# Optimization experiments

Hardware: AMD Instinct MI355X
Metric: run time of the kernel (lower is better)

The kernel has to match this reference:

```python
import jax, jax.numpy as jnp
import numpy as np

B, T, D_IN = 32, 1024, 80
SHAPES = (512, 512, 256)
WIN = 2          # delta window
H = 256          # LSTM hidden units (per direction)
LSTM_IN = SHAPES[-1] * 3


def setup_inputs() -> dict:
    key = jax.random.key(0)
    ks = jax.random.split(key, 20)
    inp = {}
    inp["x"] = jax.random.normal(ks[0], (B, T, D_IN), dtype=jnp.float32)
    lens = jax.random.randint(ks[1], (B,), T // 2, T + 1)
    inp["x_lengths"] = lens.at[0].set(T)  # ensure max length == T (static output shape)
    dims = (D_IN,) + SHAPES
    for i in range(len(SHAPES)):
        s = 1.0 / np.sqrt(dims[i])
        inp[f"enc_W{i}"] = jax.random.uniform(ks[2 + i], (dims[i + 1], dims[i]), minval=-s, maxval=s, dtype=jnp.float32)
        inp[f"enc_b{i}"] = jax.random.uniform(ks[5 + i], (dims[i + 1],), minval=-s, maxval=s, dtype=jnp.float32)
    s = 1.0 / np.sqrt(H)
    for d, name in enumerate(("f", "b")):
        inp[f"W_ih_{name}"] = jax.random.uniform(ks[8 + 4 * d], (4 * H, LSTM_IN), minval=-s, maxval=s, dtype=jnp.float32)
        inp[f"W_hh_{name}"] = jax.random.uniform(ks[9 + 4 * d], (4 * H, H), minval=-s, maxval=s, dtype=jnp.float32)
        inp[f"b_ih_{name}"] = jax.random.uniform(ks[10 + 4 * d], (4 * H,), minval=-s, maxval=s, dtype=jnp.float32)
        inp[f"b_hh_{name}"] = jax.random.uniform(ks[11 + 4 * d], (4 * H,), minval=-s, maxval=s, dtype=jnp.float32)
    # init_hidden() in torch uses randn; fix it here as deterministic inputs. [2 dirs, B, H]
    inp["h0"] = jax.random.normal(ks[16], (2, B, H), dtype=jnp.float32)
    inp["c0"] = jax.random.normal(ks[17], (2, B, H), dtype=jnp.float32)
    return inp


def _deltas(x, w):
    # edge-replicated window, z[:,t] = sum_j (y[t+w+j]-y[t+w-j])/(2j)
    Tt = x.shape[1]
    y = jnp.concatenate([jnp.repeat(x[:, :1], w, axis=1), x, jnp.repeat(x[:, -1:], w, axis=1)], axis=1)
    z = jnp.zeros_like(x)
    for j in range(1, w + 1):
        z = z + (y[:, w + j:w + j + Tt] - y[:, w - j:w - j + Tt]) / (2.0 * j)
    return z


def _lstm(xs, h0, c0, Wih, Whh, b):
    # xs: [T, B, F] -> hs: [T, B, H]; torch gate order i,f,g,o
    def step(carry, xt):
        h, c = carry
        g = xt @ Wih.T + h @ Whh.T + b
        i, f, gg, o = jnp.split(g, 4, axis=-1)
        c = jax.nn.sigmoid(f) * c + jax.nn.sigmoid(i) * jnp.tanh(gg)
        h = jax.nn.sigmoid(o) * jnp.tanh(c)
        return (h, c), h
    _, hs = jax.lax.scan(step, (h0, c0), xs)
    return hs


def _forward(x, x_lengths, enc_W0, enc_b0, enc_W1, enc_b1, enc_W2, enc_b2,
             W_ih_f, W_hh_f, b_ih_f, b_hh_f, W_ih_b, W_hh_b, b_ih_b, b_hh_b, h0, c0):
    # MLP encoder with ReLU after every layer
    h = x
    for Wm, bm in ((enc_W0, enc_b0), (enc_W1, enc_b1), (enc_W2, enc_b2)):
        h = jax.nn.relu(h @ Wm.T + bm)
    d1 = _deltas(h, WIN)
    d2 = _deltas(d1, WIN)
    feat = jnp.concatenate([h, d1, d2], axis=2)  # [B, T, 3*shapes[-1]]
    # sort by length descending (pack_padded_sequence)
    order = jnp.argsort(-x_lengths)
    lens = x_lengths[order]
    feat = feat[order]
    t_idx = jnp.arange(T)
    # forward direction
    hf = _lstm(jnp.swapaxes(feat, 0, 1), h0[0], c0[0], W_ih_f, W_hh_f, b_ih_f + b_hh_f)
    hf = jnp.swapaxes(hf, 0, 1)  # [B, T, H]
    # backward direction: reverse valid part of each sequence (packed semantics)
    rev = jnp.clip(lens[:, None] - 1 - t_idx[None, :], 0, T - 1)  # [B, T]
    x_rev = jnp.take_along_axis(feat, rev[:, :, None], axis=1)
    hb = _lstm(jnp.swapaxes(x_rev, 0, 1), h0[1], c0[1], W_ih_b, W_hh_b, b_ih_b + b_hh_b)
    hb = jnp.take_along_axis(jnp.swapaxes(hb, 0, 1), rev[:, :, None], axis=1)
    # pad_packed_sequence zeros out padded steps
    mask = (t_idx[None, :] < lens[:, None])[:, :, None]
    out = jnp.where(mask, jnp.concatenate([hf, hb], axis=2), 0.0)
    return out, order


def reference(x, x_lengths, enc_W0, enc_b0, enc_W1, enc_b1, enc_W2, enc_b2,
              W_ih_f, W_hh_f, b_ih_f, b_hh_f, W_ih_b, W_hh_b, b_ih_b, b_hh_b, h0, c0):
    return _forward(x, x_lengths, enc_W0, enc_b0, enc_W1, enc_b1, enc_W2, enc_b2,
                    W_ih_f, W_hh_f, b_ih_f, b_hh_f, W_ih_b, W_hh_b, b_ih_b, b_hh_b, h0, c0)
```

## Files before the change

### kernel.cpp

```cpp
#include <hip/hip_runtime.h>
#include <cstdint>
#include <cstddef>

#define B_SZ 32
#define T_SZ 1024
#define DIN  80
#define H3   256
#define FEAT 768
#define G4   1024
#define HH   256

typedef __attribute__((ext_vector_type(8))) short short8;
typedef __attribute__((ext_vector_type(4))) float f32x4;
typedef __attribute__((ext_vector_type(8))) int v8i;

__device__ inline float bf2f(unsigned short u) {
    return __uint_as_float(((unsigned int)u) << 16);
}
__device__ inline unsigned short f2bf(float f) {
    unsigned int u = __float_as_uint(f);
    u += 0x7fffu + ((u >> 16) & 1u);
    return (unsigned short)(u >> 16);
}
#define LOG2E 1.4426950408889634f
__device__ inline float sigm(float x) {
    return __builtin_amdgcn_rcpf(1.f + __builtin_amdgcn_exp2f(x * -LOG2E));
}
__device__ inline float tanh_f(float x) {
    return fmaf(2.f, __builtin_amdgcn_rcpf(1.f + __builtin_amdgcn_exp2f(x * (-2.f * LOG2E))), -1.f);
}

__device__ inline void gld16(const void* g, void* l) {
    __builtin_amdgcn_global_load_lds(
        (const __attribute__((address_space(1))) unsigned int*)g,
        (__attribute__((address_space(3))) unsigned int*)l, 16, 0, 0);
}

__device__ inline void cvt_seg(const float* __restrict__ s, unsigned short* __restrict__ d,
                               int n4, int i, int stride) {
    for (int k = i; k < n4; k += stride) {
        float4 f = ((const float4*)(const void*)s)[k];
        ushort4 u;
        u.x = f2bf(f.x); u.y = f2bf(f.y); u.z = f2bf(f.z); u.w = f2bf(f.w);
        ((ushort4*)(void*)d)[k] = u;
    }
}

__global__ void k_cvt4(const float* __restrict__ src, unsigned short* __restrict__ dst, int n4) {
    int i = blockIdx.x * 256 + threadIdx.x;
    cvt_seg(src, dst, n4, i, gridDim.x * 256);
}

__global__ void k_cvtw(const float* __restrict__ s0, unsigned short* __restrict__ d0,
                       const float* __restrict__ s1, unsigned short* __restrict__ d1,
                       const float* __restrict__ s2, unsigned short* __restrict__ d2,
                       const float* __restrict__ s3, unsigned short* __restrict__ d3,
                       const float* __restrict__ s4, unsigned short* __restrict__ d4) {
    int i = blockIdx.x * 256 + threadIdx.x;
    int stride = gridDim.x * 256;
    cvt_seg(s0, d0, 10240,  i, stride);
    cvt_seg(s1, d1, 65536,  i, stride);
    cvt_seg(s2, d2, 32768,  i, stride);
    cvt_seg(s3, d3, 196608, i, stride);
    cvt_seg(s4, d4, 196608, i, stride);
}

__global__ void k_order(const int* __restrict__ lens, int* __restrict__ order,
                        int* __restrict__ lens_sorted, float* __restrict__ out_order) {
    int b = threadIdx.x;
    if (b < B_SZ) {
        int lb = lens[b];
        int r = 0;
        for (int j = 0; j < B_SZ; ++j) {
            int lj = lens[j];
            if (lj > lb || (lj == lb && j < b)) ++r;
        }
        order[r] = b;
        lens_sorted[r] = lb;
        out_order[r] = (float)b;
    }
}

__global__ void k_ztail(const int* __restrict__ lens_sorted, float* __restrict__ out) {
    int t = blockIdx.x, bs = blockIdx.y;
    if (t < lens_sorted[bs]) return;
    float4* p = (float4*)(out + ((size_t)bs * T_SZ + t) * 512);
    p[threadIdx.x] = make_float4(0.f, 0.f, 0.f, 0.f);
}

__global__ void k_wfrag8(const float* __restrict__ Whhf, const float* __restrict__ Whhb,
                         unsigned char* __restrict__ dst) {
    int t = blockIdx.x * 256 + threadIdx.x;
    int dir = t >> 14;
    t &= 16383;
    const float* Whh = dir ? Whhb : Whhf;
    unsigned char* d = dst + (size_t)dir * 262144;
    int lane = t & 63, hf = (t >> 6) & 1, kc = (t >> 7) & 1, nt = t >> 8;
    int l16 = lane & 15;
    int gb = nt >> 4, m = nt & 15, wv = m >> 1, pp = m & 1;
    int n = gb * 256 + wv * 32 + l16 * 2 + pp;
    int k0 = kc * 128 + (lane >> 4) * 32 + hf * 16;
    const float* p = Whh + (size_t)n * 256 + k0;
    unsigned int o[4];
    #pragma unroll
    for (int q = 0; q < 4; ++q) {
        float4 f = *(const float4*)(const void*)(p + 4 * q);
        o[q] = (__builtin_amdgcn_cvt_pk_fp8_f32(f.x, f.y, 0, false) & 0xffff)
             | (__builtin_amdgcn_cvt_pk_fp8_f32(f.z, f.w, 0, false) << 16);
    }
    int slot = (nt * 2 + kc) * 64 + lane;
    *(uint4*)(void*)(d + (size_t)slot * 32 + hf * 16) = make_uint4(o[0], o[1], o[2], o[3]);
}

__global__ __launch_bounds__(256) void k_gemm(
    const unsigned short* __restrict__ A, const unsigned short* __restrict__ Bw,
    const float* __restrict__ bias1, const float* __restrict__ bias2,
    unsigned short* __restrict__ C, int M, int N, int K, int relu)
{
    int tid  = threadIdx.x;
    int lane = tid & 63;
    int wave = tid >> 6;
    int waveM = wave >> 1, waveN = wave & 1;
    int l16  = lane & 15;
    int quad = lane >> 4;
    int mBase = blockIdx.x * 32 + waveM * 16;
    int nBase = blockIdx.y * 128 + waveN * 64;

    const unsigned short* pA  = A  + (size_t)(mBase + l16) * K + quad * 8;
    const unsigned short* pB0 = Bw + (size_t)(nBase +  0 + l16) * K + quad * 8;
    const unsigned short* pB1 = Bw + (size_t)(nBase + 16 + l16) * K + quad * 8;
    const unsigned short* pB2 = Bw + (size_t)(nBase + 32 + l16) * K + quad * 8;
    const unsigned short* pB3 = Bw + (size_t)(nBase + 48 + l16) * K + quad * 8;

    const short8 z8 = {0, 0, 0, 0, 0, 0, 0, 0};
    f32x4 acc0 = {0.f, 0.f, 0.f, 0.f};
    f32x4 acc1 = acc0, acc2 = acc0, acc3 = acc0;

    for (int k0 = 0; k0 < K; k0 += 32) {
        bool ok = (k0 + quad * 8) < K;
        short8 av  = ok ? *(const short8*)(const void*)(pA  + k0) : z8;
        short8 bv0 = ok ? *(const short8*)(const void*)(pB0 + k0) : z8;
        short8 bv1 = ok ? *(const short8*)(const void*)(pB1 + k0) : z8;
        short8 bv2 = ok ? *(const short8*)(const void*)(pB2 + k0) : z8;
        short8 bv3 = ok ? *(const short8*)(const void*)(pB3 + k0) : z8;
        acc0 = __builtin_amdgcn_mfma_f32_16x16x32_bf16(av, bv0, acc0, 0, 0, 0);
        acc1 = __builtin_amdgcn_mfma_f32_16x16x32_bf16(av, bv1, acc1, 0, 0, 0);
        acc2 = __builtin_amdgcn_mfma_f32_16x16x32_bf16(av, bv2, acc2, 0, 0, 0);
        acc3 = __builtin_amdgcn_mfma_f32_16x16x32_bf16(av, bv3, acc3, 0, 0, 0);
    }

    int rowD = mBase + quad * 4;
    #pragma unroll
    for (int nt = 0; nt < 4; ++nt) {
        int col = nBase + nt * 16 + l16;
        float bsum = 0.f;
        if (bias1) bsum += bias1[col];
        if (bias2) bsum += bias2[col];
        f32x4 a = (nt == 0) ? acc0 : (nt == 1) ? acc1 : (nt == 2) ? acc2 : acc3;
        #pragma unroll
        for (int r = 0; r < 4; ++r) {
            float v = a[r] + bsum;
            if (relu) v = v > 0.f ? v : 0.f;
            C[(size_t)(rowD + r) * N + col] = f2bf(v);
        }
    }
}

__global__ __launch_bounds__(256) void k_gemm_t(
    const unsigned short* __restrict__ A, const unsigned short* __restrict__ Bw,
    const float* __restrict__ bias1, const float* __restrict__ bias2,
    unsigned short* __restrict__ C, int N, int K, int relu)
{
    __shared__ unsigned short lA[128 * 32];
    __shared__ unsigned short lB[128 * 32];
    int tid  = threadIdx.x;
    int lane = tid & 63;
    int wave = tid >> 6;
    int l16  = lane & 15, quad = lane >> 4;
    int wm = wave >> 1, wn = wave & 1;
    size_t mBase = (size_t)blockIdx.y * 128;
    size_t nBase = (size_t)blockIdx.x * 128;

    int c0 = tid, c1 = tid + 256;
    const unsigned short* sA0 = A  + (mBase + (c0 >> 2)) * K + (c0 & 3) * 8;
    const unsigned short* sA1 = A  + (mBase + (c1 >> 2)) * K + (c1 & 3) * 8;
    const unsigned short* sB0 = Bw + (nBase + (c0 >> 2)) * K + (c0 & 3) * 8;
    const unsigned short* sB1 = Bw + (nBase + (c1 >> 2)) * K + (c1 & 3) * 8;
    unsigned short* dA0 = lA + c0 * 8;
    unsigned short* dA1 = lA + c1 * 8;
    unsigned short* dB0 = lB + c0 * 8;
    unsigned short* dB1 = lB + c1 * 8;

    f32x4 acc[4][4];
    #pragma unroll
    for (int i = 0; i < 4; ++i)
        #pragma unroll
        for (int j = 0; j < 4; ++j) acc[i][j] = (f32x4){0.f, 0.f, 0.f, 0.f};

    const unsigned short* la = lA + (wm * 64 + l16) * 32 + quad * 8;
    const unsigned short* lb = lB + (wn * 64 + l16) * 32 + quad * 8;

    for (int k0 = 0; k0 < K; k0 += 32) {
        gld16(sA0 + k0, dA0);
        gld16(sA1 + k0, dA1);
        gld16(sB0 + k0, dB0);
        gld16(sB1 + k0, dB1);
        __syncthreads();
        short8 af[4], bf[4];
        #pragma unroll
        for (int i = 0; i < 4; ++i) {
            af[i] = *(const short8*)(const void*)(la + i * 16 * 32);
            bf[i] = *(const short8*)(const void*)(lb + i * 16 * 32);
        }
        #pragma unroll
        for (int i = 0; i < 4; ++i)
            #pragma unroll
            for (int j = 0; j < 4; ++j)
                acc[i][j] = __builtin_amdgcn_mfma_f32_16x16x32_bf16(af[i], bf[j], acc[i][j], 0, 0, 0);
        __syncthreads();
    }

    #pragma unroll
    for (int j = 0; j < 4; ++j) {
        int col = (int)nBase + wn * 64 + j * 16 + l16;
        float bsum = 0.f;
        if (bias1) bsum += bias1[col];
        if (bias2) bsum += bias2[col];
        #pragma unroll
        for (int i = 0; i < 4; ++i) {
            int row = (int)mBase + wm * 64 + i * 16 + quad * 4;
            #pragma unroll
            for (int r = 0; r < 4; ++r) {
                float v = acc[i][j][r] + bsum;
                if (relu) v = v > 0.f ? v : 0.f;
                C[(size_t)(row + r) * N + col] = f2bf(v);
            }
        }
    }
}

__global__ void k_deltas(const unsigned short* __restrict__ hbuf, const int* __restrict__ order,
                         unsigned short* __restrict__ feat)
{
    int bt = blockIdx.x;
    int c  = threadIdx.x;
    int bs = bt >> 10, t = bt & 1023;
    int b  = order[bs];
    const unsigned short* hb = hbuf + (size_t)b * T_SZ * H3 + c;

    float hv[9];
    #pragma unroll
    for (int d = -4; d <= 4; ++d) {
        int tt = t + d;
        tt = tt < 0 ? 0 : (tt > T_SZ - 1 ? T_SZ - 1 : tt);
        hv[d + 4] = bf2f(hb[(size_t)tt * H3]);
    }
    float d1v[5];
    #pragma unroll
    for (int s = -2; s <= 2; ++s) {
        d1v[s + 2] = (hv[s + 5] - hv[s + 3]) * 0.5f + (hv[s + 6] - hv[s + 2]) * 0.25f;
    }
    int sp1 = (t + 1 > T_SZ - 1 ? T_SZ - 1 : t + 1) - t;
    int sm1 = (t - 1 < 0 ? 0 : t - 1) - t;
    int sp2 = (t + 2 > T_SZ - 1 ? T_SZ - 1 : t + 2) - t;
    int sm2 = (t - 2 < 0 ? 0 : t - 2) - t;
    float d2 = (d1v[2 + sp1] - d1v[2 + sm1]) * 0.5f + (d1v[2 + sp2] - d1v[2 + sm2]) * 0.25f;

    size_t fb = (size_t)bt * FEAT;
    feat[fb + c]       = hb[(size_t)t * H3];
    feat[fb + 256 + c] = f2bf(d1v[2]);
    feat[fb + 512 + c] = f2bf(d2);
}

__global__ __launch_bounds__(512, 2) void k_lstm_fp8(
    const unsigned short* __restrict__ g3f, const unsigned short* __restrict__ g3b,
    const unsigned char* __restrict__ wfrag8,
    const float* __restrict__ h0, const float* __restrict__ c0,
    const int* __restrict__ lens_sorted, float* __restrict__ out)
{
    int rq = blockIdx.x, dir = blockIdx.y;
    const unsigned short* g3 = (dir ? g3b : g3f) + (size_t)rq * 4194304;
    const unsigned char* wsrc = wfrag8 + (size_t)dir * 262144;

    __shared__ __align__(16) unsigned char hA[2][4096];

    int tid = threadIdx.x;
    int wave = tid >> 6, lane = tid & 63;
    int l16 = lane & 15, quad = lane >> 4;

    v8i regB[4][2][2];
    #pragma unroll
    for (int gb = 0; gb < 4; ++gb)
        #pragma unroll
        for (int p = 0; p < 2; ++p)
            #pragma unroll
            for (int kc = 0; kc < 2; ++kc) {
                int nt = gb * 16 + 2 * wave + p;
                regB[gb][p][kc] = *(const v8i*)(const void*)
                    (wsrc + ((size_t)((nt * 2 + kc) * 64 + lane)) * 32);
            }

    for (int i = tid; i < 2048; i += 512) ((unsigned int*)(void*)hA)[i] = 0;
    __syncthreads();
    for (int i = tid; i < 1024; i += 512) {
        int b = i >> 8, c = i & 255;
        float hv = h0[(size_t)dir * B_SZ * HH + (size_t)(rq * 4 + b) * HH + c];
        hA[0][(c >> 7) * 2048 + (((c >> 5) & 3) * 16 + 4 * b) * 32 + (c & 31)] =
            (unsigned char)(__builtin_amdgcn_cvt_pk_fp8_f32(hv, hv, 0, false) & 0xff);
    }

    int grow = rq * 4 + quad;
    int elen = lens_sorted[grow];
    int maxlen = lens_sorted[rq * 4];
    int col0 = 32 * wave + 2 * l16;
    float2 cini = *(const float2*)(const void*)
        (c0 + (size_t)dir * B_SZ * HH + (size_t)grow * HH + col0);
    float c2[2] = {cini.x, cini.y};
    float* out_r = out + (size_t)grow * T_SZ * 512 + dir * HH + col0;
    const unsigned short* gbase0 = g3 + ((size_t)quad << 20) + col0;
    int woff = (col0 >> 7) * 2048 + (((col0 >> 5) & 3) * 16 + 4 * quad) * 32 + (col0 & 31);

    {
        int tr0 = dir ? (elen - 1) : 0;
        const unsigned short* rp = gbase0 + ((size_t)tr0 << 10);
        unsigned int t0 = *(const unsigned int*)(const void*)(rp);
        unsigned int t1 = *(const unsigned int*)(const void*)(rp + 256);
        unsigned int t2 = *(const unsigned int*)(const void*)(rp + 512);
        unsigned int t3 = *(const unsigned int*)(const void*)(rp + 768);
        __syncthreads();

        unsigned int gI = t0, gF = t1, gG = t2, gO = t3;
        const f32x4 zf = {0.f, 0.f, 0.f, 0.f};

        for (int s = 0; s < maxlen; ++s) {
            const unsigned char* Ab = hA[s & 1];
            v8i a0 = *(const v8i*)(const void*)(Ab + lane * 32);
            v8i a1 = *(const v8i*)(const void*)(Ab + 2048 + lane * 32);

            int trn = dir ? (elen - 2 - s) : (s + 1);
            trn = trn < 0 ? 0 : (trn > T_SZ - 1 ? T_SZ - 1 : trn);
            const unsigned short* rn = gbase0 + ((size_t)trn << 10);
            unsigned int nI = *(const unsigned int*)(const void*)(rn);
            unsigned int nF = *(const unsigned int*)(const void*)(rn + 256);
            unsigned int nG = *(const unsigned int*)(const void*)(rn + 512);
            unsigned int nO = *(const unsigned int*)(const void*)(rn + 768);

            f32x4 acc[4][2];
            #pragma unroll
            for (int gb = 0; gb < 4; ++gb)
                #pragma unroll
                for (int p = 0; p < 2; ++p)
                    acc[gb][p] = __builtin_amdgcn_mfma_scale_f32_16x16x128_f8f6f4(
                        a0, regB[gb][p][0], zf, 0, 0, 0, 0x7F7F7F7F, 0, 0x7F7F7F7F);
            #pragma unroll
            for (int gb = 0; gb < 4; ++gb)
                #pragma unroll
                for (int p = 0; p < 2; ++p)
                    acc[gb][p] = __builtin_amdgcn_mfma_scale_f32_16x16x128_f8f6f4(
                        a1, regB[gb][p][1], acc[gb][p], 0, 0, 0, 0x7F7F7F7F, 0, 0x7F7F7F7F);

            float tc[2];
            #pragma unroll
            for (int p = 0; p < 2; ++p) {
                float iv = acc[0][p][0] + bf2f((unsigned short)(p ? (gI >> 16) : (gI & 0xffffu)));
                float fv = acc[1][p][0] + bf2f((unsigned short)(p ? (gF >> 16) : (gF & 0xffffu)));
                float gv = acc[2][p][0] + bf2f((unsigned short)(p ? (gG >> 16) : (gG & 0xffffu)));
                c2[p] = sigm(fv) * c2[p] + sigm(iv) * tanh_f(gv);
                tc[p] = tanh_f(c2[p]);
            }
            float ov0 = acc[3][0][0] + bf2f((unsigned short)(gO & 0xffffu));
            float ov1 = acc[3][1][0] + bf2f((unsigned short)(gO >> 16));
            float hv0 = sigm(ov0) * tc[0];
            float hv1 = sigm(ov1) * tc[1];

            unsigned short pk = (unsigned short)
                (__builtin_amdgcn_cvt_pk_fp8_f32(hv0, hv1, 0, false) & 0xffffu);
            *(unsigned short*)(void*)(hA[(s + 1) & 1] + woff) = pk;
            if (s < elen) {
                int t_out = dir ? (elen - 1 - s) : s;
                *(float2*)(void*)(out_r + (size_t)t_out * 512) = make_float2(hv0, hv1);
            }
            gI = nI; gF = nF; gG = nG; gO = nO;
            asm volatile("s_waitcnt lgkmcnt(0)" ::: "memory");
            __builtin_amdgcn_s_barrier();
        }
    }
}

#define OFF_XBF    ((size_t)0)
#define OFF_A0     ((size_t)5242880)
#define OFF_A1     ((size_t)38797312)
#define OFF_HBUF   ((size_t)72351744)
#define OFF_FEAT   ((size_t)89128960)
#define OFF_GF     OFF_A0
#define OFF_GB     ((size_t)139460608)
#define OFF_W0     ((size_t)206569472)
#define OFF_W1     ((size_t)206651392)
#define OFF_W2     ((size_t)207175680)
#define OFF_WIHF   ((size_t)207437824)
#define OFF_WIHB   ((size_t)209010688)
#define OFF_WFRAG  ((size_t)210583552)
#define OFF_ORDER  ((size_t)212680704)
#define OFF_LENS   ((size_t)212680832)

extern "C" void kernel_launch(void* const* d_in, const int* in_sizes, int n_in,
                              void* d_out, int out_size, void* d_ws, size_t ws_size,
                              hipStream_t stream)
{
    const float* x    = (const float*)d_in[0];
    const int*   xlen = (const int*)d_in[1];
    const float* eW0  = (const float*)d_in[2];
    const float* eb0  = (const float*)d_in[3];
    const float* eW1  = (const float*)d_in[4];
    const float* eb1  = (const float*)d_in[5];
    const float* eW2  = (const float*)d_in[6];
    const float* eb2  = (const float*)d_in[7];
    const float* Wihf = (const float*)d_in[8];
    const float* Whhf = (const float*)d_in[9];
    const float* bihf = (const float*)d_in[10];
    const float* bhhf = (const float*)d_in[11];
    const float* Wihb = (const float*)d_in[12];
    const float* Whhb = (const float*)d_in[13];
    const float* bihb = (const float*)d_in[14];
    const float* bhhb = (const float*)d_in[15];
    const float* h0   = (const float*)d_in[16];
    const float* c0   = (const float*)d_in[17];
    float* out = (float*)d_out;

    char* ws = (char*)d_ws;
    unsigned short* xbf    = (unsigned short*)(ws + OFF_XBF);
    unsigned short* a0     = (unsigned short*)(ws + OFF_A0);
    unsigned short* a1     = (unsigned short*)(ws + OFF_A1);
    unsigned short* hbuf   = (unsigned short*)(ws + OFF_HBUF);
    unsigned short* feat   = (unsigned short*)(ws + OFF_FEAT);
    unsigned short* gatesF = (unsigned short*)(ws + OFF_GF);
    unsigned short* gatesB = (unsigned short*)(ws + OFF_GB);
    unsigned short* w0     = (unsigned short*)(ws + OFF_W0);
    unsigned short* w1     = (unsigned short*)(ws + OFF_W1);
    unsigned short* w2     = (unsigned short*)(ws + OFF_W2);
    unsigned short* wihf   = (unsigned short*)(ws + OFF_WIHF);
    unsigned short* wihb   = (unsigned short*)(ws + OFF_WIHB);
    unsigned char*  wfrag8 = (unsigned char*)(ws + OFF_WFRAG);
    int* order             = (int*)(ws + OFF_ORDER);
    int* lens_sorted       = (int*)(ws + OFF_LENS);

    k_cvt4<<<1024, 256, 0, stream>>>(x, xbf, B_SZ * T_SZ * DIN / 4);
    k_cvtw<<<512, 256, 0, stream>>>(eW0, w0, eW1, w1, eW2, w2, Wihf, wihf, Wihb, wihb);
    k_wfrag8<<<128, 256, 0, stream>>>(Whhf, Whhb, wfrag8);
    k_order<<<1, 64, 0, stream>>>(xlen, order, lens_sorted, out + (size_t)B_SZ * T_SZ * 512);
    k_ztail<<<dim3(T_SZ, B_SZ), 128, 0, stream>>>(lens_sorted, out);

    k_gemm<<<dim3(1024, 4), 256, 0, stream>>>(xbf, w0, nullptr, eb0, a0, 32768, 512, 80, 1);
    k_gemm_t<<<dim3(4, 256), 256, 0, stream>>>(a0, w1, eb1, nullptr, a1,   512, 512, 1);
    k_gemm_t<<<dim3(2, 256), 256, 0, stream>>>(a1, w2, eb2, nullptr, hbuf, 256, 512, 1);

    k_deltas<<<32768, 256, 0, stream>>>(hbuf, order, feat);

    k_gemm_t<<<dim3(8, 256), 256, 0, stream>>>(feat, wihf, bihf, bhhf, gatesF, 1024, 768, 0);
    k_gemm_t<<<dim3(8, 256), 256, 0, stream>>>(feat, wihb, bihb, bhhb, gatesB, 1024, 768, 0);

    k_lstm_fp8<<<dim3(8, 2), 512, 0, stream>>>(gatesF, gatesB, wfrag8, h0, c0,
                                               lens_sorted, out);
}
```

Baseline: 1.236 ms.

## Widen LSTM recurrence to 1024 threads and merge setup and input-gate GEMMs

The recurrent LSTM kernel now runs 16 waves per block, each owning one 16-column tile per gate instead of two. The precomputed input gates are fed in as the MFMA accumulator initialiser rather than added afterwards. The Whh fragment layout is simplified to match the new per-wave ownership. The x conversion, bias summation and length sorting are folded into one setup kernel, and the forward and backward input-projection GEMMs run as a single launch over N=2048, which assumes wihb sits contiguously after wihf in the workspace. The aim is to shorten the serial per-step critical path and cut launch count, at the cost of more threads joining each barrier and more register pressure at 1024 threads per block.

```diff
diff --git a/kernel.cpp b/kernel.cpp
--- a/kernel.cpp
+++ b/kernel.cpp
@@ -46,38 +46,37 @@
     }
 }
 
-__global__ void k_cvt4(const float* __restrict__ src, unsigned short* __restrict__ dst, int n4) {
-    int i = blockIdx.x * 256 + threadIdx.x;
-    cvt_seg(src, dst, n4, i, gridDim.x * 256);
-}
-
-__global__ void k_cvtw(const float* __restrict__ s0, unsigned short* __restrict__ d0,
+__global__ void k_cvtw(const float* __restrict__ x,  unsigned short* __restrict__ xbf,
+                       const float* __restrict__ s0, unsigned short* __restrict__ d0,
                        const float* __restrict__ s1, unsigned short* __restrict__ d1,
                        const float* __restrict__ s2, unsigned short* __restrict__ d2,
                        const float* __restrict__ s3, unsigned short* __restrict__ d3,
-                       const float* __restrict__ s4, unsigned short* __restrict__ d4) {
+                       const float* __restrict__ s4, unsigned short* __restrict__ d4,
+                       const float* __restrict__ bihf, const float* __restrict__ bhhf,
+                       const float* __restrict__ bihb, const float* __restrict__ bhhb,
+                       float* __restrict__ bsum,
+                       const int* __restrict__ lens, int* __restrict__ order,
+                       int* __restrict__ lens_sorted, float* __restrict__ out_order) {
     int i = blockIdx.x * 256 + threadIdx.x;
     int stride = gridDim.x * 256;
+    cvt_seg(x,  xbf, 655360, i, stride);
     cvt_seg(s0, d0, 10240,  i, stride);
     cvt_seg(s1, d1, 65536,  i, stride);
     cvt_seg(s2, d2, 32768,  i, stride);
     cvt_seg(s3, d3, 196608, i, stride);
     cvt_seg(s4, d4, 196608, i, stride);
-}
-
-__global__ void k_order(const int* __restrict__ lens, int* __restrict__ order,
-                        int* __restrict__ lens_sorted, float* __restrict__ out_order) {
-    int b = threadIdx.x;
-    if (b < B_SZ) {
-        int lb = lens[b];
+    if (i < 2048)
+        bsum[i] = (i < 1024) ? (bihf[i] + bhhf[i]) : (bihb[i - 1024] + bhhb[i - 1024]);
+    if (i < B_SZ) {
+        int lb = lens[i];
         int r = 0;
         for (int j = 0; j < B_SZ; ++j) {
             int lj = lens[j];
-            if (lj > lb || (lj == lb && j < b)) ++r;
-        }
-        order[r] = b;
+            if (lj > lb || (lj == lb && j < i)) ++r;
+        }
+        order[r] = i;
         lens_sorted[r] = lb;
-        out_order[r] = (float)b;
+        out_order[r] = (float)i;
     }
 }
 
@@ -96,9 +95,7 @@
     const float* Whh = dir ? Whhb : Whhf;
     unsigned char* d = dst + (size_t)dir * 262144;
     int lane = t & 63, hf = (t >> 6) & 1, kc = (t >> 7) & 1, nt = t >> 8;
-    int l16 = lane & 15;
-    int gb = nt >> 4, m = nt & 15, wv = m >> 1, pp = m & 1;
-    int n = gb * 256 + wv * 32 + l16 * 2 + pp;
+    int n = nt * 16 + (lane & 15);
     int k0 = kc * 128 + (lane >> 4) * 32 + hf * 16;
     const float* p = Whh + (size_t)n * 256 + k0;
     unsigned int o[4];
@@ -114,7 +111,7 @@
 
 __global__ __launch_bounds__(256) void k_gemm(
     const unsigned short* __restrict__ A, const unsigned short* __restrict__ Bw,
-    const float* __restrict__ bias1, const float* __restrict__ bias2,
+    const float* __restrict__ bias,
     unsigned short* __restrict__ C, int M, int N, int K, int relu)
 {
     int tid  = threadIdx.x;
@@ -153,9 +150,7 @@
     #pragma unroll
     for (int nt = 0; nt < 4; ++nt) {
         int col = nBase + nt * 16 + l16;
-        float bsum = 0.f;
-        if (bias1) bsum += bias1[col];
-        if (bias2) bsum += bias2[col];
+        float bsum = bias ? bias[col] : 0.f;
         f32x4 a = (nt == 0) ? acc0 : (nt == 1) ? acc1 : (nt == 2) ? acc2 : acc3;
         #pragma unroll
         for (int r = 0; r < 4; ++r) {
@@ -168,8 +163,9 @@
 
 __global__ __launch_bounds__(256) void k_gemm_t(
     const unsigned short* __restrict__ A, const unsigned short* __restrict__ Bw,
-    const float* __restrict__ bias1, const float* __restrict__ bias2,
-    unsigned short* __restrict__ C, int N, int K, int relu)
+    const float* __restrict__ bias,
+    unsigned short* __restrict__ C, unsigned short* __restrict__ C2,
+    int N, int K, int ldc, int relu)
 {
     __shared__ unsigned short lA[128 * 32];
     __shared__ unsigned short lB[128 * 32];
@@ -222,10 +218,11 @@
 
     #pragma unroll
     for (int j = 0; j < 4; ++j) {
-        int col = (int)nBase + wn * 64 + j * 16 + l16;
-        float bsum = 0.f;
-        if (bias1) bsum += bias1[col];
-        if (bias2) bsum += bias2[col];
+        int colg = (int)nBase + wn * 64 + j * 16 + l16;
+        float bsum = bias[colg];
+        unsigned short* dst = C;
+        int cg = colg;
+        if (C2 && colg >= 1024) { dst = C2; cg = colg - 1024; }
         #pragma unroll
         for (int i = 0; i < 4; ++i) {
             int row = (int)mBase + wm * 64 + i * 16 + quad * 4;
@@ -233,7 +230,7 @@
             for (int r = 0; r < 4; ++r) {
                 float v = acc[i][j][r] + bsum;
                 if (relu) v = v > 0.f ? v : 0.f;
-                C[(size_t)(row + r) * N + col] = f2bf(v);
+                dst[(size_t)(row + r) * ldc + cg] = f2bf(v);
             }
         }
     }
@@ -272,7 +269,7 @@
     feat[fb + 512 + c] = f2bf(d2);
 }
 
-__global__ __launch_bounds__(512, 2) void k_lstm_fp8(
+__global__ __launch_bounds__(1024, 4) void k_lstm_fp8(
     const unsigned short* __restrict__ g3f, const unsigned short* __restrict__ g3b,
     const unsigned char* __restrict__ wfrag8,
     const float* __restrict__ h0, const float* __restrict__ c0,
@@ -285,25 +282,23 @@
     __shared__ __align__(16) unsigned char hA[2][4096];
 
     int tid = threadIdx.x;
-    int wave = tid >> 6, lane = tid & 63;
+    int w = tid >> 6, lane = tid & 63;
     int l16 = lane & 15, quad = lane >> 4;
 
-    v8i regB[4][2][2];
+    v8i regB[4][2];
     #pragma unroll
     for (int gb = 0; gb < 4; ++gb)
         #pragma unroll
-        for (int p = 0; p < 2; ++p)
-            #pragma unroll
-            for (int kc = 0; kc < 2; ++kc) {
-                int nt = gb * 16 + 2 * wave + p;
-                regB[gb][p][kc] = *(const v8i*)(const void*)
-                    (wsrc + ((size_t)((nt * 2 + kc) * 64 + lane)) * 32);
-            }
-
-    for (int i = tid; i < 2048; i += 512) ((unsigned int*)(void*)hA)[i] = 0;
+        for (int kc = 0; kc < 2; ++kc) {
+            int nt = gb * 16 + w;
+            regB[gb][kc] = *(const v8i*)(const void*)
+                (wsrc + ((size_t)((nt * 2 + kc) * 64 + lane)) * 32);
+        }
+
+    for (int i = tid; i < 2048; i += 1024) ((unsigned int*)(void*)hA)[i] = 0;
     __syncthreads();
-    for (int i = tid; i < 1024; i += 512) {
-        int b = i >> 8, c = i & 255;
+    {
+        int b = tid >> 8, c = tid & 255;
         float hv = h0[(size_t)dir * B_SZ * HH + (size_t)(rq * 4 + b) * HH + c];
         hA[0][(c >> 7) * 2048 + (((c >> 5) & 3) * 16 + 4 * b) * 32 + (c & 31)] =
             (unsigned char)(__builtin_amdgcn_cvt_pk_fp8_f32(hv, hv, 0, false) & 0xff);
@@ -312,78 +307,54 @@
     int grow = rq * 4 + quad;
     int elen = lens_sorted[grow];
     int maxlen = lens_sorted[rq * 4];
-    int col0 = 32 * wave + 2 * l16;
-    float2 cini = *(const float2*)(const void*)
-        (c0 + (size_t)dir * B_SZ * HH + (size_t)grow * HH + col0);
-    float c2[2] = {cini.x, cini.y};
-    float* out_r = out + (size_t)grow * T_SZ * 512 + dir * HH + col0;
-    const unsigned short* gbase0 = g3 + ((size_t)quad << 20) + col0;
-    int woff = (col0 >> 7) * 2048 + (((col0 >> 5) & 3) * 16 + 4 * quad) * 32 + (col0 & 31);
-
-    {
-        int tr0 = dir ? (elen - 1) : 0;
-        const unsigned short* rp = gbase0 + ((size_t)tr0 << 10);
-        unsigned int t0 = *(const unsigned int*)(const void*)(rp);
-        unsigned int t1 = *(const unsigned int*)(const void*)(rp + 256);
-        unsigned int t2 = *(const unsigned int*)(const void*)(rp + 512);
-        unsigned int t3 = *(const unsigned int*)(const void*)(rp + 768);
-        __syncthreads();
-
-        unsigned int gI = t0, gF = t1, gG = t2, gO = t3;
-        const f32x4 zf = {0.f, 0.f, 0.f, 0.f};
-
-        for (int s = 0; s < maxlen; ++s) {
-            const unsigned char* Ab = hA[s & 1];
-            v8i a0 = *(const v8i*)(const void*)(Ab + lane * 32);
-            v8i a1 = *(const v8i*)(const void*)(Ab + 2048 + lane * 32);
-
-            int trn = dir ? (elen - 2 - s) : (s + 1);
-            trn = trn < 0 ? 0 : (trn > T_SZ - 1 ? T_SZ - 1 : trn);
-            const unsigned short* rn = gbase0 + ((size_t)trn << 10);
-            unsigned int nI = *(const unsigned int*)(const void*)(rn);
-            unsigned int nF = *(const unsigned int*)(const void*)(rn + 256);
-            unsigned int nG = *(const unsigned int*)(const void*)(rn + 512);
-            unsigned int nO = *(const unsigned int*)(const void*)(rn + 768);
-
-            f32x4 acc[4][2];
-            #pragma unroll
-            for (int gb = 0; gb < 4; ++gb)
-                #pragma unroll
-                for (int p = 0; p < 2; ++p)
-                    acc[gb][p] = __builtin_amdgcn_mfma_scale_f32_16x16x128_f8f6f4(
-                        a0, regB[gb][p][0], zf, 0, 0, 0, 0x7F7F7F7F, 0, 0x7F7F7F7F);
-            #pragma unroll
-            for (int gb = 0; gb < 4; ++gb)
-                #pragma unroll
-                for (int p = 0; p < 2; ++p)
-                    acc[gb][p] = __builtin_amdgcn_mfma_scale_f32_16x16x128_f8f6f4(
-                        a1, regB[gb][p][1], acc[gb][p], 0, 0, 0, 0x7F7F7F7F, 0, 0x7F7F7F7F);
-
-            float tc[2];
-            #pragma unroll
-            for (int p = 0; p < 2; ++p) {
-                float iv = acc[0][p][0] + bf2f((unsigned short)(p ? (gI >> 16) : (gI & 0xffffu)));
-                float fv = acc[1][p][0] + bf2f((unsigned short)(p ? (gF >> 16) : (gF & 0xffffu)));
-                float gv = acc[2][p][0] + bf2f((unsigned short)(p ? (gG >> 16) : (gG & 0xffffu)));
-                c2[p] = sigm(fv) * c2[p] + sigm(iv) * tanh_f(gv);
-                tc[p] = tanh_f(c2[p]);
-            }
-            float ov0 = acc[3][0][0] + bf2f((unsigned short)(gO & 0xffffu));
-            float ov1 = acc[3][1][0] + bf2f((unsigned short)(gO >> 16));
-            float hv0 = sigm(ov0) * tc[0];
-            float hv1 = sigm(ov1) * tc[1];
-
-            unsigned short pk = (unsigned short)
-                (__builtin_amdgcn_cvt_pk_fp8_f32(hv0, hv1, 0, false) & 0xffffu);
-            *(unsigned short*)(void*)(hA[(s + 1) & 1] + woff) = pk;
-            if (s < elen) {
-                int t_out = dir ? (elen - 1 - s) : s;
-                *(float2*)(void*)(out_r + (size_t)t_out * 512) = make_float2(hv0, hv1);
-            }
-            gI = nI; gF = nF; gG = nG; gO = nO;
-            asm volatile("s_waitcnt lgkmcnt(0)" ::: "memory");
-            __builtin_amdgcn_s_barrier();
-        }
+    int col = w * 16 + l16;
+    float c2 = c0[(size_t)dir * B_SZ * HH + (size_t)grow * HH + col];
+    float* out_r = out + (size_t)grow * T_SZ * 512 + dir * HH + col;
+    const unsigned short* gb0 = g3 + ((size_t)quad << 20) + col;
+    int woff = (col >> 7) * 2048 + (((col >> 5) & 3) * 16 + 4 * quad) * 32 + (col & 31);
+
+    int tr0 = dir ? (elen - 1) : 0;
+    const unsigned short* rp = gb0 + ((size_t)tr0 << 10);
+    unsigned short gI = rp[0], gF = rp[256], gG = rp[512], gO = rp[768];
+    __syncthreads();
+
+    for (int s = 0; s < maxlen; ++s) {
+        const unsigned char* Ab = hA[s & 1];
+        v8i a0 = *(const v8i*)(const void*)(Ab + lane * 32);
+        v8i a1 = *(const v8i*)(const void*)(Ab + 2048 + lane * 32);
+
+        int trn = dir ? (elen - 2 - s) : (s + 1);
+        trn = trn < 0 ? 0 : (trn > T_SZ - 1 ? T_SZ - 1 : trn);
+        const unsigned short* rn = gb0 + ((size_t)trn << 10);
+        unsigned short nI = rn[0], nF = rn[256], nG = rn[512], nO = rn[768];
+
+        f32x4 acc[4];
+        acc[0] = (f32x4){bf2f(gI), 0.f, 0.f, 0.f};
+        acc[1] = (f32x4){bf2f(gF), 0.f, 0.f, 0.f};
+        acc[2] = (f32x4){bf2f(gG), 0.f, 0.f, 0.f};
+        acc[3] = (f32x4){bf2f(gO), 0.f, 0.f, 0.f};
+        #pragma unroll
+        for (int gb = 0; gb < 4; ++gb)
+            acc[gb] = __builtin_amdgcn_mfma_scale_f32_16x16x128_f8f6f4(
+                a0, regB[gb][0], acc[gb], 0, 0, 0, 0x7F7F7F7F, 0, 0x7F7F7F7F);
+        #pragma unroll
+        for (int gb = 0; gb < 4; ++gb)
+            acc[gb] = __builtin_amdgcn_mfma_scale_f32_16x16x128_f8f6f4(
+                a1, regB[gb][1], acc[gb], 0, 0, 0, 0x7F7F7F7F, 0, 0x7F7F7F7F);
+
+        c2 = sigm(acc[1][0]) * c2 + sigm(acc[0][0]) * tanh_f(acc[2][0]);
+        float tc = tanh_f(c2);
+        float hv = sigm(acc[3][0]) * tc;
+
+        hA[(s + 1) & 1][woff] =
+            (unsigned char)(__builtin_amdgcn_cvt_pk_fp8_f32(hv, hv, 0, false) & 0xff);
+        if (s < elen) {
+            int t_out = dir ? (elen - 1 - s) : s;
+            out_r[(size_t)t_out * 512] = hv;
+        }
+        gI = nI; gF = nF; gG = nG; gO = nO;
+        asm volatile("s_waitcnt lgkmcnt(0)" ::: "memory");
+        __builtin_amdgcn_s_barrier();
     }
 }
 
@@ -400,6 +371,7 @@
 #define OFF_WIHF   ((size_t)207437824)
 #define OFF_WIHB   ((size_t)209010688)
 #define OFF_WFRAG  ((size_t)210583552)
+#define OFF_BSUM   ((size_t)211107840)
 #define OFF_ORDER  ((size_t)212680704)
 #define OFF_LENS   ((size_t)212680832)
 
@@ -441,24 +413,27 @@
     unsigned short* wihf   = (unsigned short*)(ws + OFF_WIHF);
     unsigned short* wihb   = (unsigned short*)(ws + OFF_WIHB);
     unsigned char*  wfrag8 = (unsigned char*)(ws + OFF_WFRAG);
+    float* bsum            = (float*)(ws + OFF_BSUM);
     int* order             = (int*)(ws + OFF_ORDER);
     int* lens_sorted       = (int*)(ws + OFF_LENS);
 
-    k_cvt4<<<1024, 256, 0, stream>>>(x, xbf, B_SZ * T_SZ * DIN / 4);
-    k_cvtw<<<512, 256, 0, stream>>>(eW0, w0, eW1, w1, eW2, w2, Wihf, wihf, Wihb, wihb);
+    k_cvtw<<<1024, 256, 0, stream>>>(x, xbf, eW0, w0, eW1, w1, eW2, w2,
+                                     Wihf, wihf, Wihb, wihb,
+                                     bihf, bhhf, bihb, bhhb, bsum,
+                                     xlen, order, lens_sorted,
+                                     out + (size_t)B_SZ * T_SZ * 512);
     k_wfrag8<<<128, 256, 0, stream>>>(Whhf, Whhb, wfrag8);
-    k_order<<<1, 64, 0, stream>>>(xlen, order, lens_sorted, out + (size_t)B_SZ * T_SZ * 512);
     k_ztail<<<dim3(T_SZ, B_SZ), 128, 0, stream>>>(lens_sorted, out);
 
-    k_gemm<<<dim3(1024, 4), 256, 0, stream>>>(xbf, w0, nullptr, eb0, a0, 32768, 512, 80, 1);
-    k_gemm_t<<<dim3(4, 256), 256, 0, stream>>>(a0, w1, eb1, nullptr, a1,   512, 512, 1);
-    k_gemm_t<<<dim3(2, 256), 256, 0, stream>>>(a1, w2, eb2, nullptr, hbuf, 256, 512, 1);
+    k_gemm<<<dim3(1024, 4), 256, 0, stream>>>(xbf, w0, eb0, a0, 32768, 512, 80, 1);
+    k_gemm_t<<<dim3(4, 256), 256, 0, stream>>>(a0, w1, eb1, a1,   nullptr, 512, 512, 512, 1);
+    k_gemm_t<<<dim3(2, 256), 256, 0, stream>>>(a1, w2, eb2, hbuf, nullptr, 256, 512, 256, 1);
 
     k_deltas<<<32768, 256, 0, stream>>>(hbuf, order, feat);
 
-    k_gemm_t<<<dim3(8, 256), 256, 0, stream>>>(feat, wihf, bihf, bhhf, gatesF, 1024, 768, 0);
-    k_gemm_t<<<dim3(8, 256), 256, 0, stream>>>(feat, wihb, bihb, bhhb, gatesB, 1024, 768, 0);
-
-    k_lstm_fp8<<<dim3(8, 2), 512, 0, stream>>>(gatesF, gatesB, wfrag8, h0, c0,
-                                               lens_sorted, out);
-}
+    k_gemm_t<<<dim3(16, 256), 256, 0, stream>>>(feat, wihf, bsum, gatesF, gatesB,
+                                                2048, 768, 1024, 0);
+
+    k_lstm_fp8<<<dim3(8, 2), 1024, 0, stream>>>(gatesF, gatesB, wfrag8, h0, c0,
+                                                lens_sorted, out);
+}
```

New measurement: 1.215 ms. No clear change (-1.7%).
